# Performance work log

Measured on AMD Instinct MI355X. Metric: run time of the kernel, lower is better.

The kernel has to match this reference:

```python
import jax, jax.numpy as jnp
import numpy as np

N = 5000        # nodes
F = 7699        # node feature dim (fixed by code)
E = 40000       # edges
ED = 3          # edge_dim (fixed by code)
H1, C1 = 4, 1024
H2, C2 = 1, 1024
NUM_OUT = 128
NEG_SLOPE = 0.2


def _glorot(key, shape):
    fan_in = shape[0]
    return jax.random.normal(key, shape, jnp.float32) / np.float32(np.sqrt(fan_in))


def setup_inputs() -> dict:
    key = jax.random.key(0)
    ks = jax.random.split(key, 16)
    x = jax.random.normal(ks[0], (N, F), jnp.float32)
    src = jax.random.randint(ks[1], (E,), 0, N)
    dst = jax.random.randint(ks[2], (E,), 0, N)
    src = jnp.where(src == dst, (src + 1) % N, src)  # no pre-existing self loops
    edge_index = jnp.stack([src, dst]).astype(jnp.int32)
    edge_attr = jax.random.normal(ks[3], (E, ED), jnp.float32)
    inp = {
        "x": x, "edge_index": edge_index, "edge_attr": edge_attr,
        # GATv2Conv #1: 7699 -> 1024, heads=4, edge_dim=3
        "W1l": _glorot(ks[4], (F, H1 * C1)), "b1l": jnp.zeros((H1 * C1,), jnp.float32),
        "W1r": _glorot(ks[5], (F, H1 * C1)), "b1r": jnp.zeros((H1 * C1,), jnp.float32),
        "W1e": _glorot(ks[6], (ED, H1 * C1)),
        "att1": _glorot(ks[7], (H1, C1)),
        "bias1": jnp.zeros((H1 * C1,), jnp.float32),
        # GATv2Conv #2: 4096 -> 1024, heads=1, edge_dim=3
        "W2l": _glorot(ks[8], (H1 * C1, H2 * C2)), "b2l": jnp.zeros((H2 * C2,), jnp.float32),
        "W2r": _glorot(ks[9], (H1 * C1, H2 * C2)), "b2r": jnp.zeros((H2 * C2,), jnp.float32),
        "W2e": _glorot(ks[10], (ED, H2 * C2)),
        "att2": _glorot(ks[11], (H2, C2)),
        "bias2": jnp.zeros((H2 * C2,), jnp.float32),
        # final Linear(1024, num_outputs)
        "Wlin": _glorot(ks[12], (C2, NUM_OUT)), "blin": jnp.zeros((NUM_OUT,), jnp.float32),
    }
    return inp


def gatv2_layer(x, src, dst, edge_attr, Wl, bl, Wr, br, We, att, bias, heads, out_ch):
    """PyG GATv2Conv with add_self_loops=True, fill_value='mean', concat=True."""
    n = x.shape[0]
    # self-loop edge_attr = mean of incoming edge attrs per node (fill_value='mean')
    deg = jax.ops.segment_sum(jnp.ones((src.shape[0],), jnp.float32), dst, num_segments=n)
    loop_attr = jax.ops.segment_sum(edge_attr, dst, num_segments=n) / jnp.maximum(deg, 1.0)[:, None]
    idx = jnp.arange(n, dtype=src.dtype)
    srcf = jnp.concatenate([src, idx])
    dstf = jnp.concatenate([dst, idx])
    ea = jnp.concatenate([edge_attr, loop_attr], axis=0)
    xl = (x @ Wl + bl).reshape(n, heads, out_ch)   # lin_l (source)
    xr = (x @ Wr + br).reshape(n, heads, out_ch)   # lin_r (target)
    ee = (ea @ We).reshape(-1, heads, out_ch)       # lin_edge (no bias)
    e = jax.nn.leaky_relu(xl[srcf] + xr[dstf] + ee, NEG_SLOPE)  # [E', H, C]
    logit = jnp.einsum('ehc,hc->eh', e, att)                     # [E', H]
    # segment softmax over destination nodes (every node has a self loop)
    m = jax.lax.stop_gradient(jax.ops.segment_max(logit, dstf, num_segments=n))
    a = jnp.exp(logit - m[dstf])
    denom = jax.ops.segment_sum(a, dstf, num_segments=n)
    alpha = a / (denom[dstf] + 1e-16)
    out = jax.ops.segment_sum(alpha[:, :, None] * xl[srcf], dstf, num_segments=n)  # [N,H,C]
    return out.reshape(n, heads * out_ch) + bias


def reference(x, edge_index, edge_attr,
              W1l, b1l, W1r, b1r, W1e, att1, bias1,
              W2l, b2l, W2r, b2r, W2e, att2, bias2,
              Wlin, blin):
    src, dst = edge_index[0], edge_index[1]
    h = gatv2_layer(x, src, dst, edge_attr, W1l, b1l, W1r, b1r, W1e, att1, bias1, H1, C1)
    h = gatv2_layer(h, src, dst, edge_attr, W2l, b2l, W2r, b2r, W2e, att2, bias2, H2, C2)
    return h @ Wlin + blin
```

## Files before the change

kernel.cpp:

```cpp
#include <hip/hip_runtime.h>
#include <cstdint>
#include <cstddef>

#define N_NODES 5000
#define F_IN    7699
#define KP1     7712
#define KT1     241
#define MP      5120
#define E_EDGES 40000
#define EFULL   45000
#define HC1     4096
#define N1      8192
#define HC2     1024
#define N2      2048
#define NOUT    128
#define GM      (MP / 256)

typedef __bf16 bf16x8 __attribute__((ext_vector_type(8)));
typedef float  f32x4  __attribute__((ext_vector_type(4)));
typedef float  f32x16 __attribute__((ext_vector_type(16)));
typedef unsigned short u16x8 __attribute__((ext_vector_type(8)));
typedef _Float16 f16;
typedef _Float16 f16x8 __attribute__((ext_vector_type(8)));

using as1_uchar = unsigned char __attribute__((address_space(1)));
using as3_uchar = unsigned char __attribute__((address_space(3)));

__device__ __forceinline__ unsigned short f2bf(float f) {
  union { float f; unsigned int u; } v; v.f = f;
  return (unsigned short)((v.u + 0x7fffu + ((v.u >> 16) & 1u)) >> 16);
}
__device__ __forceinline__ float bf2f(unsigned short h) {
  union { unsigned int u; float f; } v; v.u = ((unsigned int)h) << 16;
  return v.f;
}

__device__ __forceinline__ void gload16(const void* g, void* l) {
  __builtin_amdgcn_global_load_lds(
      reinterpret_cast<const as1_uchar*>(reinterpret_cast<uintptr_t>(g)),
      reinterpret_cast<as3_uchar*>(reinterpret_cast<uintptr_t>(l)),
      16, 0, 0);
}



__global__ void k_split_x(const float* __restrict__ x, unsigned short* __restrict__ hi,
                          unsigned short* __restrict__ lo) {
  const int C8 = KP1 / 8;
  int ci = blockIdx.x * 256 + threadIdx.x;
  if (ci >= MP * C8) return;
  int r = ci / C8, c8 = ci % C8;
  int c = c8 * 8;
  u16x8 hb, lb;
  #pragma unroll
  for (int j = 0; j < 8; ++j) {
    float v = 0.f;
    if (r < N_NODES && (c + j) < F_IN) v = x[(size_t)r * F_IN + c + j];
    unsigned short h = f2bf(v);
    hb[j] = h; lb[j] = f2bf(v - bf2f(h));
  }
  size_t off = ((size_t)((r >> 7) * KT1 + (c >> 5)) * 4 + ((c >> 3) & 3)) * 1024 + (r & 127) * 8;
  *(u16x8*)&hi[off] = hb;
  *(u16x8*)&lo[off] = lb;
}


__global__ void k_split_w(const float* __restrict__ W,
                          unsigned short* __restrict__ hi, unsigned short* __restrict__ lo,
                          int K, int Nsrc, int c0, int KT, int rowOffset) {
  __shared__ float tile[32][33];
  const int tid = threadIdx.x;
  const int kt = blockIdx.x;
  const int n0 = blockIdx.y * 32;
  #pragma unroll
  for (int i = tid >> 5; i < 32; i += 8) {
    int k = kt * 32 + i;
    tile[i][tid & 31] = (k < K) ? W[(size_t)k * Nsrc + c0 + n0 + (tid & 31)] : 0.f;
  }
  __syncthreads();
  if (tid < 128) {
    const int nn = tid >> 2, kc = (tid & 3) << 3;
    const int n = rowOffset + n0 + nn;
    u16x8 hb, lb;
    #pragma unroll
    for (int j = 0; j < 8; ++j) {
      float v = tile[kc + j][nn];
      unsigned short h = f2bf(v);
      hb[j] = h; lb[j] = f2bf(v - bf2f(h));
    }
    size_t off = ((size_t)((n >> 7) * KT + kt) * 4 + (kc >> 3)) * 1024 + (n & 127) * 8;
    *(u16x8*)&hi[off] = hb;
    *(u16x8*)&lo[off] = lb;
  }
}


template <int OF16>
__global__ __launch_bounds__(512, 2) void k_gemm_bb(
    const unsigned short* __restrict__ Ahi, const unsigned short* __restrict__ Alo,
    const unsigned short* __restrict__ Bhi, const unsigned short* __restrict__ Blo,
    void* __restrict__ Cp, const float* __restrict__ bias0, const float* __restrict__ bias1,
    int halfN, int M, int ldC, int KT, int gm)
{
  __shared__ __align__(16) unsigned short S[3 * 24576];

  const int tid = threadIdx.x;
  const int lane = tid & 63;
  const int w = tid >> 6;
  const int wm = w >> 1, wn = w & 1;

  const int nwg = gridDim.x;
  const int qq = nwg >> 3, rr = nwg & 7;
  const int xcd = blockIdx.x & 7, idx = blockIdx.x >> 3;
  const int wg = (xcd < rr ? xcd * (qq + 1) : rr * (qq + 1) + (xcd - rr) * qq) + idx;
  const int bn = wg / gm, bm = wg % gm;

  f32x16 acc[2][2] = {};

  const size_t aoff = (size_t)(2 * bm) * KT * 4096 + w * 512 + lane * 8;
  const unsigned short* b0 = Ahi + aoff;
  const unsigned short* b1 = b0 + (size_t)KT * 4096;
  const unsigned short* b2 = Alo + aoff;
  const unsigned short* b3 = b2 + (size_t)KT * 4096;
  const unsigned short* b4 = Bhi + (size_t)bn * KT * 4096 + w * 512 + lane * 8;
  const unsigned short* b5 = Blo + (size_t)bn * KT * 4096 + w * 512 + lane * 8;
  const int ldst = w * 512;

  auto stage = [&](int kt, int bufo) {
    const size_t o = (size_t)kt * 4096;
    gload16(b0 + o, &S[bufo + 0 * 4096 + ldst]);
    gload16(b1 + o, &S[bufo + 1 * 4096 + ldst]);
    gload16(b2 + o, &S[bufo + 2 * 4096 + ldst]);
    gload16(b3 + o, &S[bufo + 3 * 4096 + ldst]);
    gload16(b4 + o, &S[bufo + 4 * 4096 + ldst]);
    gload16(b5 + o, &S[bufo + 5 * 4096 + ldst]);
  };

  const int r5 = lane & 31, h5 = lane >> 5;
  const int arow0 = wm * 64 + r5;
  const int arow1 = arow0 + 32;
  const int at[2]  = { arow0 >> 7, arow1 >> 7 };
  const int ar[2]  = { (arow0 & 127) * 8, (arow1 & 127) * 8 };
  const int bc[2]  = { (wn * 64 + r5) * 8, (wn * 64 + 32 + r5) * 8 };
  const int pl = h5 * 1024;

  stage(0, 0);
  stage(1, 24576);
  asm volatile("s_waitcnt vmcnt(6)" ::: "memory");
  __builtin_amdgcn_s_barrier();

  int ocur = 0, onxt = 24576, onx2 = 49152;
  for (int kt = 0; kt < KT; ++kt) {
    const int ks = (kt + 2 < KT) ? kt + 2 : KT - 1;
    stage(ks, onx2);

    bf16x8 ah[2][2], al[2][2], bh[2][2], bl[2][2];
    #pragma unroll
    for (int i = 0; i < 2; ++i)
      #pragma unroll
      for (int kh = 0; kh < 2; ++kh) {
        const int po = ocur + kh * 2048 + pl;
        ah[i][kh] = *(const bf16x8*)&S[po + at[i] * 4096 + ar[i]];
        al[i][kh] = *(const bf16x8*)&S[po + (2 + at[i]) * 4096 + ar[i]];
      }
    #pragma unroll
    for (int j = 0; j < 2; ++j)
      #pragma unroll
      for (int kh = 0; kh < 2; ++kh) {
        const int po = ocur + kh * 2048 + pl;
        bh[j][kh] = *(const bf16x8*)&S[po + 4 * 4096 + bc[j]];
        bl[j][kh] = *(const bf16x8*)&S[po + 5 * 4096 + bc[j]];
      }

    __builtin_amdgcn_s_setprio(1);
    #pragma unroll
    for (int j = 0; j < 2; ++j)
      #pragma unroll
      for (int kh = 0; kh < 2; ++kh)
        #pragma unroll
        for (int i = 0; i < 2; ++i) {
          acc[i][j] = __builtin_amdgcn_mfma_f32_32x32x16_bf16(ah[i][kh], bh[j][kh], acc[i][j], 0, 0, 0);
          acc[i][j] = __builtin_amdgcn_mfma_f32_32x32x16_bf16(al[i][kh], bh[j][kh], acc[i][j], 0, 0, 0);
          acc[i][j] = __builtin_amdgcn_mfma_f32_32x32x16_bf16(ah[i][kh], bl[j][kh], acc[i][j], 0, 0, 0);
        }
    __builtin_amdgcn_s_setprio(0);

    asm volatile("s_waitcnt vmcnt(6)" ::: "memory");
    __builtin_amdgcn_s_barrier();
    const int t = ocur; ocur = onxt; onxt = onx2; onx2 = t;
  }

  #pragma unroll
  for (int i = 0; i < 2; ++i) {
    #pragma unroll
    for (int j = 0; j < 2; ++j) {
      const int gc = bn * 128 + wn * 64 + j * 32 + r5;
      const float bv = (gc < halfN) ? bias0[gc] : bias1[gc - halfN];
      #pragma unroll
      for (int reg = 0; reg < 16; ++reg) {
        const int gr = bm * 256 + wm * 64 + i * 32 + (reg & 3) + 8 * (reg >> 2) + 4 * h5;
        if (gr < M) {
          float v = acc[i][j][reg] + bv;
          if (OF16) ((f16*)Cp)[(size_t)gr * ldC + gc] = (f16)v;
          else      ((float*)Cp)[(size_t)gr * ldC + gc] = v;
        }
      }
    }
  }
}


__global__ void k_deg(const int* __restrict__ dst, const float* __restrict__ ea,
                      float* __restrict__ deg, float* __restrict__ lattr, int E) {
  int e = blockIdx.x * 256 + threadIdx.x;
  if (e >= E) return;
  int d = dst[e];
  atomicAdd(&deg[d], 1.f);
  atomicAdd(&lattr[d * 3 + 0], ea[e * 3 + 0]);
  atomicAdd(&lattr[d * 3 + 1], ea[e * 3 + 1]);
  atomicAdd(&lattr[d * 3 + 2], ea[e * 3 + 2]);
}

__global__ void k_lattr_fin(float* __restrict__ lattr, const float* __restrict__ deg, int n) {
  int i = blockIdx.x * 256 + threadIdx.x;
  if (i >= n) return;
  float dv = fmaxf(deg[i], 1.f);
  lattr[i * 3 + 0] /= dv; lattr[i * 3 + 1] /= dv; lattr[i * 3 + 2] /= dv;
}

__global__ void k_eafull(const float* __restrict__ ea, const float* __restrict__ lattr,
                         float* __restrict__ eaf, int E, int n) {
  int e = blockIdx.x * 256 + threadIdx.x;
  if (e >= E + n) return;
  const float* s = (e < E) ? &ea[(size_t)e * 3] : &lattr[(size_t)(e - E) * 3];
  eaf[e * 3 + 0] = s[0]; eaf[e * 3 + 1] = s[1]; eaf[e * 3 + 2] = s[2];
}

__global__ void k_count(const int* __restrict__ dst, int* __restrict__ cnt, int E, int n) {
  int e = blockIdx.x * 256 + threadIdx.x;
  if (e >= E + n) return;
  int d = (e < E) ? dst[e] : (e - E);
  atomicAdd(&cnt[d], 1);
}

__global__ void k_scan(const int* __restrict__ cnt, int* __restrict__ rowptr, int n) {
  int lane = threadIdx.x;
  int run = 0;
  for (int base = 0; base < n; base += 64) {
    int i = base + lane;
    int v = (i < n) ? cnt[i] : 0;
    #pragma unroll
    for (int off = 1; off < 64; off <<= 1) {
      int t = __shfl_up(v, off, 64);
      if (lane >= off) v += t;
    }
    if (i < n) rowptr[i + 1] = run + v;
    run += __shfl(v, 63, 64);
  }
  if (lane == 0) rowptr[0] = 0;
}

__global__ void k_fill(const int* __restrict__ dst, const int* __restrict__ rowptr,
                       int* __restrict__ fillc, int* __restrict__ elist, int E, int n) {
  int e = blockIdx.x * 256 + threadIdx.x;
  if (e >= E + n) return;
  int d = (e < E) ? dst[e] : (e - E);
  int pos = rowptr[d] + atomicAdd(&fillc[d], 1);
  elist[pos] = e;
}


template <int H, int ITERS>
__global__ __launch_bounds__(256) void k_logit(
    const f16* __restrict__ xl, const f16* __restrict__ xr, int strideX,
    const float* __restrict__ eaf, const float* __restrict__ We, const float* __restrict__ att,
    const int* __restrict__ src, const int* __restrict__ dst, int E,
    float* __restrict__ logit)
{
  const int e = blockIdx.x;
  const int tid = threadIdx.x;
  int s, d;
  if (e < E) { s = src[e]; d = dst[e]; } else { s = e - E; d = s; }
  const float ea0 = eaf[e * 3 + 0], ea1 = eaf[e * 3 + 1], ea2 = eaf[e * 3 + 2];
  constexpr int HC = ITERS * 256;
  const f16* rl = xl + (size_t)s * strideX;
  const f16* rr = xr + (size_t)d * strideX;
  float acc[H];
  #pragma unroll
  for (int h = 0; h < H; ++h) acc[h] = 0.f;
  #pragma unroll
  for (int i = 0; i < ITERS; ++i) {
    int hc = tid + (i << 8);
    float v = (float)rl[hc] + (float)rr[hc]
            + ea0 * We[hc] + ea1 * We[HC + hc] + ea2 * We[2 * HC + hc];
    v = (v > 0.f) ? v : 0.2f * v;
    acc[i >> 2] += v * att[hc];
  }
  __shared__ float red[H][4];
  const int lane = tid & 63, wv = tid >> 6;
  #pragma unroll
  for (int h = 0; h < H; ++h) {
    float v = acc[h];
    #pragma unroll
    for (int off = 32; off > 0; off >>= 1) v += __shfl_down(v, off, 64);
    if (lane == 0) red[h][wv] = v;
  }
  __syncthreads();
  if (tid < H)
    logit[(size_t)e * H + tid] = red[tid][0] + red[tid][1] + red[tid][2] + red[tid][3];
}

template <int H>
__global__ void k_stats(const float* __restrict__ logit, const int* __restrict__ rowptr,
                        const int* __restrict__ elist, float* __restrict__ mb, float* __restrict__ db)
{
  const int n = blockIdx.x;
  const int lane = threadIdx.x;
  const int start = rowptr[n], end = rowptr[n + 1];
  #pragma unroll
  for (int h = 0; h < H; ++h) {
    float m = -1e30f;
    for (int p = start + lane; p < end; p += 64)
      m = fmaxf(m, logit[(size_t)elist[p] * H + h]);
    #pragma unroll
    for (int off = 32; off > 0; off >>= 1) m = fmaxf(m, __shfl_down(m, off, 64));
    m = __shfl(m, 0, 64);
    float sum = 0.f;
    for (int p = start + lane; p < end; p += 64)
      sum += __expf(logit[(size_t)elist[p] * H + h] - m);
    #pragma unroll
    for (int off = 32; off > 0; off >>= 1) sum += __shfl_down(sum, off, 64);
    if (lane == 0) { mb[n * H + h] = m; db[n * H + h] = sum; }
  }
}

template <int H, int NC8, int KTo>
__global__ __launch_bounds__(256) void k_agg(
    const f16* __restrict__ xl, int strideX,
    const int* __restrict__ rowptr, const int* __restrict__ elist, const int* __restrict__ src,
    const float* __restrict__ logit, const float* __restrict__ mb, const float* __restrict__ db,
    const float* __restrict__ bias,
    unsigned short* __restrict__ ohi, unsigned short* __restrict__ olo, int E)
{
  const int n = blockIdx.x;
  const int tid = threadIdx.x;
  constexpr int HC = H * 1024;
  float acc[NC8][8];
  #pragma unroll
  for (int q = 0; q < NC8; ++q)
    #pragma unroll
    for (int j = 0; j < 8; ++j) acc[q][j] = 0.f;
  const int start = rowptr[n], end = rowptr[n + 1];
  float mloc[H], dloc[H];
  #pragma unroll
  for (int h = 0; h < H; ++h) { mloc[h] = mb[n * H + h]; dloc[h] = db[n * H + h] + 1e-16f; }
  for (int p = start; p < end; ++p) {
    const int e = elist[p];
    const int s = (e < E) ? src[e] : (e - E);
    float al[H];
    #pragma unroll
    for (int h = 0; h < H; ++h)
      al[h] = __expf(logit[(size_t)e * H + h] - mloc[h]) / dloc[h];
    const f16* row = xl + (size_t)s * strideX;
    #pragma unroll
    for (int q = 0; q < NC8; ++q) {
      const int c8 = tid + q * 256;
      if (c8 * 8 < HC) {
        float a = (H == 4) ? ((tid & 128) ? al[2 * q + 1] : al[2 * q]) : al[0];
        f16x8 v = *(const f16x8*)(row + c8 * 8);
        #pragma unroll
        for (int j = 0; j < 8; ++j) acc[q][j] += a * (float)v[j];
      }
    }
  }
  #pragma unroll
  for (int q = 0; q < NC8; ++q) {
    const int c8 = tid + q * 256;
    if (c8 * 8 < HC) {
      u16x8 hb, lb;
      #pragma unroll
      for (int j = 0; j < 8; ++j) {
        float v = acc[q][j] + bias[c8 * 8 + j];
        unsigned short h = f2bf(v);
        hb[j] = h; lb[j] = f2bf(v - bf2f(h));
      }
      size_t off = ((size_t)((n >> 7) * KTo + (c8 >> 2)) * 4 + (c8 & 3)) * 1024 + (n & 127) * 8;
      *(u16x8*)&ohi[off] = hb;
      *(u16x8*)&olo[off] = lb;
    }
  }
}


extern "C" void kernel_launch(void* const* d_in, const int* in_sizes, int n_in,
                              void* d_out, int out_size, void* d_ws, size_t ws_size,
                              hipStream_t stream) {
  const float* x    = (const float*)d_in[0];
  const int*   eidx = (const int*)d_in[1];
  const float* eattr= (const float*)d_in[2];
  const float* W1l  = (const float*)d_in[3];
  const float* b1l  = (const float*)d_in[4];
  const float* W1r  = (const float*)d_in[5];
  const float* b1r  = (const float*)d_in[6];
  const float* W1e  = (const float*)d_in[7];
  const float* att1 = (const float*)d_in[8];
  const float* bias1= (const float*)d_in[9];
  const float* W2l  = (const float*)d_in[10];
  const float* b2l  = (const float*)d_in[11];
  const float* W2r  = (const float*)d_in[12];
  const float* b2r  = (const float*)d_in[13];
  const float* W2e  = (const float*)d_in[14];
  const float* att2 = (const float*)d_in[15];
  const float* bias2= (const float*)d_in[16];
  const float* Wlin = (const float*)d_in[17];
  const float* blin = (const float*)d_in[18];
  float* out = (float*)d_out;

  char* ws = (char*)d_ws;
  const int* srcp = eidx;
  const int* dstp = eidx + E_EDGES;

  auto alignup = [](size_t v) { return (v + 255) & ~(size_t)255; };

  size_t mo = 0;
  auto take = [&](size_t sz) { size_t r = mo; mo = alignup(mo + sz); return r; };
  const size_t oLATTR = take((size_t)N_NODES * 3 * 4);
  const size_t oDEG   = take((size_t)N_NODES * 4);
  const size_t oEAF   = take((size_t)EFULL * 3 * 4);
  const size_t oCNT   = take((size_t)N_NODES * 4);
  const size_t oROW   = take((size_t)(N_NODES + 1) * 4);
  const size_t oFILL  = take((size_t)N_NODES * 4);
  const size_t oELIST = take((size_t)EFULL * 4);
  const size_t oLOGIT = take((size_t)EFULL * 4 * 4);
  const size_t oMB    = take((size_t)N_NODES * 4 * 4);
  const size_t oDB    = take((size_t)N_NODES * 4 * 4);
  const size_t oXHI   = take((size_t)MP * KP1 * 2);
  const size_t oXLO   = take((size_t)MP * KP1 * 2);
  const size_t oXLR   = take((size_t)N_NODES * N1 * 2);
  const size_t oBH    = take((size_t)N1 * KP1 * 2);
  const size_t needSmall = oBH + (size_t)HC1 * KP1 * 2 * 2;
  const size_t needBig   = oBH + (size_t)N1 * KP1 * 2 * 2;
  if (ws_size < needSmall) return;
  const bool big = (ws_size >= needBig);
  const size_t oBL = big ? (oBH + (size_t)N1 * KP1 * 2) : (oBH + (size_t)HC1 * KP1 * 2);

  const size_t oH1HI = oXHI;
  const size_t oH1LO = oXLO;
  const size_t oXLR2 = oXLR;
  const size_t oH2HI = oXLR + 32ull * 1024 * 1024;
  const size_t oH2LO = oXLR + 48ull * 1024 * 1024;
  const size_t oB2H  = oBH;
  const size_t oB2L  = oBH + 32ull * 1024 * 1024;
  const size_t oB3H  = oBH;
  const size_t oB3L  = oBH + 1ull * 1024 * 1024;

  unsigned short* XHI  = (unsigned short*)(ws + oXHI);
  unsigned short* XLO  = (unsigned short*)(ws + oXLO);
  f16*            XLR  = (f16*)(ws + oXLR);
  unsigned short* BH   = (unsigned short*)(ws + oBH);
  unsigned short* BL   = (unsigned short*)(ws + oBL);
  float*          LATTR= (float*)(ws + oLATTR);
  float*          DEG  = (float*)(ws + oDEG);
  float*          EAF  = (float*)(ws + oEAF);
  int*            CNT  = (int*)(ws + oCNT);
  int*            ROWP = (int*)(ws + oROW);
  int*            FILLC= (int*)(ws + oFILL);
  int*            ELIST= (int*)(ws + oELIST);
  float*          LOGIT= (float*)(ws + oLOGIT);
  float*          MB   = (float*)(ws + oMB);
  float*          DB   = (float*)(ws + oDB);
  unsigned short* H1HI = (unsigned short*)(ws + oH1HI);
  unsigned short* H1LO = (unsigned short*)(ws + oH1LO);
  f16*            XLR2 = (f16*)(ws + oXLR2);
  unsigned short* H2HI = (unsigned short*)(ws + oH2HI);
  unsigned short* H2LO = (unsigned short*)(ws + oH2LO);
  unsigned short* B2H  = (unsigned short*)(ws + oB2H);
  unsigned short* B2L  = (unsigned short*)(ws + oB2L);
  unsigned short* B3H  = (unsigned short*)(ws + oB3H);
  unsigned short* B3L  = (unsigned short*)(ws + oB3L);

  hipMemsetAsync(ws + oDEG,   0, (size_t)N_NODES * 4, stream);
  hipMemsetAsync(ws + oLATTR, 0, (size_t)N_NODES * 3 * 4, stream);
  hipMemsetAsync(ws + oCNT,   0, (size_t)N_NODES * 4, stream);
  hipMemsetAsync(ws + oFILL,  0, (size_t)N_NODES * 4, stream);

  const int gE  = (E_EDGES + 255) / 256;
  const int gEF = (EFULL + 255) / 256;
  const int gN  = (N_NODES + 255) / 256;

  k_deg<<<gE, 256, 0, stream>>>(dstp, eattr, DEG, LATTR, E_EDGES);
  k_lattr_fin<<<gN, 256, 0, stream>>>(LATTR, DEG, N_NODES);
  k_eafull<<<gEF, 256, 0, stream>>>(eattr, LATTR, EAF, E_EDGES, N_NODES);
  k_count<<<gEF, 256, 0, stream>>>(dstp, CNT, E_EDGES, N_NODES);
  k_scan<<<1, 64, 0, stream>>>(CNT, ROWP, N_NODES);
  k_fill<<<gEF, 256, 0, stream>>>(dstp, ROWP, FILLC, ELIST, E_EDGES, N_NODES);

  k_split_x<<<MP * (KP1 / 8) / 256, 256, 0, stream>>>(x, XHI, XLO);

  if (big) {
    k_split_w<<<dim3(KT1, HC1 / 32), 256, 0, stream>>>(W1l, BH, BL, F_IN, HC1, 0, KT1, 0);
    k_split_w<<<dim3(KT1, HC1 / 32), 256, 0, stream>>>(W1r, BH, BL, F_IN, HC1, 0, KT1, HC1);
    k_gemm_bb<1><<<(N1 / 128) * GM, 512, 0, stream>>>(
        XHI, XLO, BH, BL, XLR, b1l, b1r, HC1, N_NODES, N1, KT1, GM);
  } else {
    k_split_w<<<dim3(KT1, HC1 / 32), 256, 0, stream>>>(W1l, BH, BL, F_IN, HC1, 0, KT1, 0);
    k_gemm_bb<1><<<(HC1 / 128) * GM, 512, 0, stream>>>(
        XHI, XLO, BH, BL, XLR, b1l, b1l, HC1, N_NODES, N1, KT1, GM);
    k_split_w<<<dim3(KT1, HC1 / 32), 256, 0, stream>>>(W1r, BH, BL, F_IN, HC1, 0, KT1, 0);
    k_gemm_bb<1><<<(HC1 / 128) * GM, 512, 0, stream>>>(
        XHI, XLO, BH, BL, XLR + HC1, b1r, b1r, HC1, N_NODES, N1, KT1, GM);
  }

  k_logit<4, 16><<<EFULL, 256, 0, stream>>>(XLR, XLR + HC1, N1, EAF, W1e, att1, srcp, dstp, E_EDGES, LOGIT);
  k_stats<4><<<N_NODES, 64, 0, stream>>>(LOGIT, ROWP, ELIST, MB, DB);
  hipMemsetAsync(ws + oH1HI, 0, (size_t)MP * HC1 * 2, stream);
  hipMemsetAsync(ws + oH1LO, 0, (size_t)MP * HC1 * 2, stream);
  k_agg<4, 2, HC1 / 32><<<N_NODES, 256, 0, stream>>>(
      XLR, N1, ROWP, ELIST, srcp, LOGIT, MB, DB, bias1, H1HI, H1LO, E_EDGES);

  k_split_w<<<dim3(HC1 / 32, HC2 / 32), 256, 0, stream>>>(W2l, B2H, B2L, HC1, HC2, 0, HC1 / 32, 0);
  k_split_w<<<dim3(HC1 / 32, HC2 / 32), 256, 0, stream>>>(W2r, B2H, B2L, HC1, HC2, 0, HC1 / 32, HC2);
  k_gemm_bb<1><<<(N2 / 128) * GM, 512, 0, stream>>>(
      H1HI, H1LO, B2H, B2L, XLR2, b2l, b2r, HC2, N_NODES, N2, HC1 / 32, GM);

  k_logit<1, 4><<<EFULL, 256, 0, stream>>>(XLR2, XLR2 + HC2, N2, EAF, W2e, att2, srcp, dstp, E_EDGES, LOGIT);
  k_stats<1><<<N_NODES, 64, 0, stream>>>(LOGIT, ROWP, ELIST, MB, DB);
  hipMemsetAsync(ws + oH2HI, 0, (size_t)MP * HC2 * 2, stream);
  hipMemsetAsync(ws + oH2LO, 0, (size_t)MP * HC2 * 2, stream);
  k_agg<1, 1, HC2 / 32><<<N_NODES, 256, 0, stream>>>(
      XLR2, N2, ROWP, ELIST, srcp, LOGIT, MB, DB, bias2, H2HI, H2LO, E_EDGES);

  k_split_w<<<dim3(HC2 / 32, NOUT / 32), 256, 0, stream>>>(Wlin, B3H, B3L, HC2, NOUT, 0, HC2 / 32, 0);
  k_gemm_bb<0><<<(NOUT / 128) * GM, 512, 0, stream>>>(
      H2HI, H2LO, B3H, B3L, out, blin, blin, NOUT, N_NODES, NOUT, HC2 / 32, GM);
}
```

Measured before the change: 2.935 ms.

## Enlarge GEMM tile to 256x256 with 16-wide K stages and bm-major ordering

The split-bf16 GEMM kernel now computes 256x256 output tiles per workgroup instead of 256x128. Each wave holds a 4x2 grid of 32x32 accumulators, and each pipeline stage loads a K=16 slice, which shrinks the shared-memory buffers. The larger tile halves how often the A operand is re-read relative to B and raises MFMA work per LDS load. Block ordering becomes bm-major. The small-workspace fallback path is dropped, and the final 128-wide GEMM now needs zero-padded B buffers, with a column guard at the epilogue.

```diff
diff --git a/kernel.cpp b/kernel.cpp
--- a/kernel.cpp
+++ b/kernel.cpp
@@ -100,109 +100,103 @@
     const unsigned short* __restrict__ Ahi, const unsigned short* __restrict__ Alo,
     const unsigned short* __restrict__ Bhi, const unsigned short* __restrict__ Blo,
     void* __restrict__ Cp, const float* __restrict__ bias0, const float* __restrict__ bias1,
-    int halfN, int M, int ldC, int KT, int gm)
+    int halfN, int M, int Nc, int ldC, int KT32, int nbn)
 {
-  __shared__ __align__(16) unsigned short S[3 * 24576];
+  __shared__ __align__(16) unsigned short S[3 * 16384];
 
   const int tid = threadIdx.x;
   const int lane = tid & 63;
   const int w = tid >> 6;
-  const int wm = w >> 1, wn = w & 1;
+  const int wm = w >> 2, wn = w & 3;
 
   const int nwg = gridDim.x;
   const int qq = nwg >> 3, rr = nwg & 7;
   const int xcd = blockIdx.x & 7, idx = blockIdx.x >> 3;
   const int wg = (xcd < rr ? xcd * (qq + 1) : rr * (qq + 1) + (xcd - rr) * qq) + idx;
-  const int bn = wg / gm, bm = wg % gm;
-
-  f32x16 acc[2][2] = {};
-
-  const size_t aoff = (size_t)(2 * bm) * KT * 4096 + w * 512 + lane * 8;
-  const unsigned short* b0 = Ahi + aoff;
-  const unsigned short* b1 = b0 + (size_t)KT * 4096;
-  const unsigned short* b2 = Alo + aoff;
-  const unsigned short* b3 = b2 + (size_t)KT * 4096;
-  const unsigned short* b4 = Bhi + (size_t)bn * KT * 4096 + w * 512 + lane * 8;
-  const unsigned short* b5 = Blo + (size_t)bn * KT * 4096 + w * 512 + lane * 8;
-  const int ldst = w * 512;
+  const int bm = wg / nbn, bn = wg % nbn;
+
+  f32x16 acc[4][2] = {};
+
+  const int st = (w >> 2) & 1, sp = (w >> 1) & 1, sh = w & 1;
+  const size_t laneoff = (size_t)sp * 1024 + sh * 512 + lane * 8;
+  const unsigned short* gAh = Ahi + (size_t)(bm * 2 + st) * KT32 * 4096 + laneoff;
+  const unsigned short* gAl = Alo + (size_t)(bm * 2 + st) * KT32 * 4096 + laneoff;
+  const unsigned short* gBh = Bhi + (size_t)(bn * 2 + st) * KT32 * 4096 + laneoff;
+  const unsigned short* gBl = Blo + (size_t)(bn * 2 + st) * KT32 * 4096 + laneoff;
+  const int dA = (st * 2 + sp) * 1024 + sh * 512;
 
   auto stage = [&](int kt, int bufo) {
-    const size_t o = (size_t)kt * 4096;
-    gload16(b0 + o, &S[bufo + 0 * 4096 + ldst]);
-    gload16(b1 + o, &S[bufo + 1 * 4096 + ldst]);
-    gload16(b2 + o, &S[bufo + 2 * 4096 + ldst]);
-    gload16(b3 + o, &S[bufo + 3 * 4096 + ldst]);
-    gload16(b4 + o, &S[bufo + 4 * 4096 + ldst]);
-    gload16(b5 + o, &S[bufo + 5 * 4096 + ldst]);
+    const size_t o = (size_t)kt * 2048;
+    gload16(gAh + o, &S[bufo + dA]);
+    gload16(gAl + o, &S[bufo + 4096 + dA]);
+    gload16(gBh + o, &S[bufo + 8192 + dA]);
+    gload16(gBl + o, &S[bufo + 12288 + dA]);
   };
 
   const int r5 = lane & 31, h5 = lane >> 5;
-  const int arow0 = wm * 64 + r5;
-  const int arow1 = arow0 + 32;
-  const int at[2]  = { arow0 >> 7, arow1 >> 7 };
-  const int ar[2]  = { (arow0 & 127) * 8, (arow1 & 127) * 8 };
-  const int bc[2]  = { (wn * 64 + r5) * 8, (wn * 64 + 32 + r5) * 8 };
-  const int pl = h5 * 1024;
+  const int pA = (wm * 2 + h5) * 1024;
+  const int pB = 8192 + ((wn >> 1) * 2 + h5) * 1024;
+  int ra[4], cb[2];
+  #pragma unroll
+  for (int i = 0; i < 4; ++i) ra[i] = pA + (i * 32 + r5) * 8;
+  #pragma unroll
+  for (int j = 0; j < 2; ++j) cb[j] = pB + ((wn & 1) * 64 + j * 32 + r5) * 8;
+
+  const int KT16 = KT32 * 2;
 
   stage(0, 0);
-  stage(1, 24576);
-  asm volatile("s_waitcnt vmcnt(6)" ::: "memory");
+  stage(1, 16384);
+  asm volatile("s_waitcnt vmcnt(4)" ::: "memory");
   __builtin_amdgcn_s_barrier();
 
-  int ocur = 0, onxt = 24576, onx2 = 49152;
-  for (int kt = 0; kt < KT; ++kt) {
-    const int ks = (kt + 2 < KT) ? kt + 2 : KT - 1;
+  int ocur = 0, onxt = 16384, onx2 = 32768;
+  for (int kt = 0; kt < KT16; ++kt) {
+    const int ks = (kt + 2 < KT16) ? kt + 2 : KT16 - 1;
     stage(ks, onx2);
 
-    bf16x8 ah[2][2], al[2][2], bh[2][2], bl[2][2];
-    #pragma unroll
-    for (int i = 0; i < 2; ++i)
-      #pragma unroll
-      for (int kh = 0; kh < 2; ++kh) {
-        const int po = ocur + kh * 2048 + pl;
-        ah[i][kh] = *(const bf16x8*)&S[po + at[i] * 4096 + ar[i]];
-        al[i][kh] = *(const bf16x8*)&S[po + (2 + at[i]) * 4096 + ar[i]];
-      }
+    bf16x8 ah[4], al[4], bh[2], bl[2];
+    #pragma unroll
+    for (int i = 0; i < 4; ++i) {
+      ah[i] = *(const bf16x8*)&S[ocur + ra[i]];
+      al[i] = *(const bf16x8*)&S[ocur + 4096 + ra[i]];
+    }
+    #pragma unroll
+    for (int j = 0; j < 2; ++j) {
+      bh[j] = *(const bf16x8*)&S[ocur + cb[j]];
+      bl[j] = *(const bf16x8*)&S[ocur + 4096 + cb[j]];
+    }
+
+    __builtin_amdgcn_s_setprio(1);
     #pragma unroll
     for (int j = 0; j < 2; ++j)
       #pragma unroll
-      for (int kh = 0; kh < 2; ++kh) {
-        const int po = ocur + kh * 2048 + pl;
-        bh[j][kh] = *(const bf16x8*)&S[po + 4 * 4096 + bc[j]];
-        bl[j][kh] = *(const bf16x8*)&S[po + 5 * 4096 + bc[j]];
+      for (int i = 0; i < 4; ++i) {
+        acc[i][j] = __builtin_amdgcn_mfma_f32_32x32x16_bf16(ah[i], bh[j], acc[i][j], 0, 0, 0);
+        acc[i][j] = __builtin_amdgcn_mfma_f32_32x32x16_bf16(al[i], bh[j], acc[i][j], 0, 0, 0);
+        acc[i][j] = __builtin_amdgcn_mfma_f32_32x32x16_bf16(ah[i], bl[j], acc[i][j], 0, 0, 0);
       }
-
-    __builtin_amdgcn_s_setprio(1);
-    #pragma unroll
-    for (int j = 0; j < 2; ++j)
-      #pragma unroll
-      for (int kh = 0; kh < 2; ++kh)
-        #pragma unroll
-        for (int i = 0; i < 2; ++i) {
-          acc[i][j] = __builtin_amdgcn_mfma_f32_32x32x16_bf16(ah[i][kh], bh[j][kh], acc[i][j], 0, 0, 0);
-          acc[i][j] = __builtin_amdgcn_mfma_f32_32x32x16_bf16(al[i][kh], bh[j][kh], acc[i][j], 0, 0, 0);
-          acc[i][j] = __builtin_amdgcn_mfma_f32_32x32x16_bf16(ah[i][kh], bl[j][kh], acc[i][j], 0, 0, 0);
-        }
     __builtin_amdgcn_s_setprio(0);
 
-    asm volatile("s_waitcnt vmcnt(6)" ::: "memory");
+    asm volatile("s_waitcnt vmcnt(4)" ::: "memory");
     __builtin_amdgcn_s_barrier();
     const int t = ocur; ocur = onxt; onxt = onx2; onx2 = t;
   }
 
   #pragma unroll
-  for (int i = 0; i < 2; ++i) {
+  for (int i = 0; i < 4; ++i) {
     #pragma unroll
     for (int j = 0; j < 2; ++j) {
-      const int gc = bn * 128 + wn * 64 + j * 32 + r5;
-      const float bv = (gc < halfN) ? bias0[gc] : bias1[gc - halfN];
-      #pragma unroll
-      for (int reg = 0; reg < 16; ++reg) {
-        const int gr = bm * 256 + wm * 64 + i * 32 + (reg & 3) + 8 * (reg >> 2) + 4 * h5;
-        if (gr < M) {
-          float v = acc[i][j][reg] + bv;
-          if (OF16) ((f16*)Cp)[(size_t)gr * ldC + gc] = (f16)v;
-          else      ((float*)Cp)[(size_t)gr * ldC + gc] = v;
+      const int gc = bn * 256 + wn * 64 + j * 32 + r5;
+      if (gc < Nc) {
+        const float bv = (gc < halfN) ? bias0[gc] : bias1[gc - halfN];
+        #pragma unroll
+        for (int reg = 0; reg < 16; ++reg) {
+          const int gr = bm * 256 + wm * 128 + i * 32 + (reg & 3) + 8 * (reg >> 2) + 4 * h5;
+          if (gr < M) {
+            float v = acc[i][j][reg] + bv;
+            if (OF16) ((f16*)Cp)[(size_t)gr * ldC + gc] = (f16)v;
+            else      ((float*)Cp)[(size_t)gr * ldC + gc] = v;
+          }
         }
       }
     }
@@ -438,11 +432,8 @@
   const size_t oXLO   = take((size_t)MP * KP1 * 2);
   const size_t oXLR   = take((size_t)N_NODES * N1 * 2);
   const size_t oBH    = take((size_t)N1 * KP1 * 2);
-  const size_t needSmall = oBH + (size_t)HC1 * KP1 * 2 * 2;
-  const size_t needBig   = oBH + (size_t)N1 * KP1 * 2 * 2;
-  if (ws_size < needSmall) return;
-  const bool big = (ws_size >= needBig);
-  const size_t oBL = big ? (oBH + (size_t)N1 * KP1 * 2) : (oBH + (size_t)HC1 * KP1 * 2);
+  const size_t oBL    = take((size_t)N1 * KP1 * 2);
+  if (ws_size < mo) return;
 
   const size_t oH1HI = oXHI;
   const size_t oH1LO = oXLO;
@@ -496,20 +487,10 @@
   k_fill<<<gEF, 256, 0, stream>>>(dstp, ROWP, FILLC, ELIST, E_EDGES, N_NODES);
 
   k_split_x<<<MP * (KP1 / 8) / 256, 256, 0, stream>>>(x, XHI, XLO);
-
-  if (big) {
-    k_split_w<<<dim3(KT1, HC1 / 32), 256, 0, stream>>>(W1l, BH, BL, F_IN, HC1, 0, KT1, 0);
-    k_split_w<<<dim3(KT1, HC1 / 32), 256, 0, stream>>>(W1r, BH, BL, F_IN, HC1, 0, KT1, HC1);
-    k_gemm_bb<1><<<(N1 / 128) * GM, 512, 0, stream>>>(
-        XHI, XLO, BH, BL, XLR, b1l, b1r, HC1, N_NODES, N1, KT1, GM);
-  } else {
-    k_split_w<<<dim3(KT1, HC1 / 32), 256, 0, stream>>>(W1l, BH, BL, F_IN, HC1, 0, KT1, 0);
-    k_gemm_bb<1><<<(HC1 / 128) * GM, 512, 0, stream>>>(
-        XHI, XLO, BH, BL, XLR, b1l, b1l, HC1, N_NODES, N1, KT1, GM);
-    k_split_w<<<dim3(KT1, HC1 / 32), 256, 0, stream>>>(W1r, BH, BL, F_IN, HC1, 0, KT1, 0);
-    k_gemm_bb<1><<<(HC1 / 128) * GM, 512, 0, stream>>>(
-        XHI, XLO, BH, BL, XLR + HC1, b1r, b1r, HC1, N_NODES, N1, KT1, GM);
-  }
+  k_split_w<<<dim3(KT1, HC1 / 32), 256, 0, stream>>>(W1l, BH, BL, F_IN, HC1, 0, KT1, 0);
+  k_split_w<<<dim3(KT1, HC1 / 32), 256, 0, stream>>>(W1r, BH, BL, F_IN, HC1, 0, KT1, HC1);
+  k_gemm_bb<1><<<GM * (N1 / 256), 512, 0, stream>>>(
+      XHI, XLO, BH, BL, XLR, b1l, b1r, HC1, N_NODES, N1, N1, KT1, N1 / 256);
 
   k_logit<4, 16><<<EFULL, 256, 0, stream>>>(XLR, XLR + HC1, N1, EAF, W1e, att1, srcp, dstp, E_EDGES, LOGIT);
   k_stats<4><<<N_NODES, 64, 0, stream>>>(LOGIT, ROWP, ELIST, MB, DB);
@@ -520,8 +501,8 @@
 
   k_split_w<<<dim3(HC1 / 32, HC2 / 32), 256, 0, stream>>>(W2l, B2H, B2L, HC1, HC2, 0, HC1 / 32, 0);
   k_split_w<<<dim3(HC1 / 32, HC2 / 32), 256, 0, stream>>>(W2r, B2H, B2L, HC1, HC2, 0, HC1 / 32, HC2);
-  k_gemm_bb<1><<<(N2 / 128) * GM, 512, 0, stream>>>(
-      H1HI, H1LO, B2H, B2L, XLR2, b2l, b2r, HC2, N_NODES, N2, HC1 / 32, GM);
+  k_gemm_bb<1><<<GM * (N2 / 256), 512, 0, stream>>>(
+      H1HI, H1LO, B2H, B2L, XLR2, b2l, b2r, HC2, N_NODES, N2, N2, HC1 / 32, N2 / 256);
 
   k_logit<1, 4><<<EFULL, 256, 0, stream>>>(XLR2, XLR2 + HC2, N2, EAF, W2e, att2, srcp, dstp, E_EDGES, LOGIT);
   k_stats<1><<<N_NODES, 64, 0, stream>>>(LOGIT, ROWP, ELIST, MB, DB);
@@ -530,7 +511,9 @@
   k_agg<1, 1, HC2 / 32><<<N_NODES, 256, 0, stream>>>(
       XLR2, N2, ROWP, ELIST, srcp, LOGIT, MB, DB, bias2, H2HI, H2LO, E_EDGES);
 
+  hipMemsetAsync(ws + oB3H, 0, (size_t)2 * 32 * 4096 * 2, stream);
+  hipMemsetAsync(ws + oB3L, 0, (size_t)2 * 32 * 4096 * 2, stream);
   k_split_w<<<dim3(HC2 / 32, NOUT / 32), 256, 0, stream>>>(Wlin, B3H, B3L, HC2, NOUT, 0, HC2 / 32, 0);
-  k_gemm_bb<0><<<(NOUT / 128) * GM, 512, 0, stream>>>(
-      H2HI, H2LO, B3H, B3L, out, blin, blin, NOUT, N_NODES, NOUT, HC2 / 32, GM);
-}
+  k_gemm_bb<0><<<GM * 1, 512, 0, stream>>>(
+      H2HI, H2LO, B3H, B3L, out, blin, blin, NOUT, N_NODES, NOUT, NOUT, HC2 / 32, 1);
+}
```

Measured after the change: 2.886 ms. Within noise of the previous version (-1.7%).
